# Kernel tuning notes

Hardware: AMD Instinct MI355X
Metric: run time of the kernel (lower is better)

## Reference

```python
import jax, jax.numpy as jnp
import numpy as np

K = 11  # masked conv3d kernel size

def mask_A(k):
    # mask type 'A': flattened (i,j,t) positions with current_id < k^3//2 + 1
    # (current_id starts at 1) -> first k^3//2 positions are 1.
    m = (np.arange(k ** 3) < (k ** 3) // 2).astype(np.float32).reshape(k, k, k)
    return jnp.asarray(m)

def conv3d(x, w, b, pad):
    out = jax.lax.conv_general_dilated(
        x, w, window_strides=(1, 1, 1), padding=[(pad, pad)] * 3,
        dimension_numbers=('NCDHW', 'OIDHW', 'NCDHW'))
    return out + b[None, :, None, None, None]

def conv2d(x, w, b, pad):
    out = jax.lax.conv_general_dilated(
        x, w, window_strides=(1, 1), padding=[(pad, pad)] * 2,
        dimension_numbers=('NCHW', 'OIHW', 'NCHW'))
    return out + b[None, :, None, None]

def pconv(x, w, b):
    # 1x1x1 conv3d as channel GEMM; w: [O, C]
    return jnp.einsum('bcdhw,oc->bodhw', x, w) + b[None, :, None, None, None]

def _phi(z):
    return 0.5 * (1.0 + jax.lax.erf(z / jnp.sqrt(2.0).astype(z.dtype)))

def setup_inputs() -> dict:
    key = jax.random.key(0)
    ks = jax.random.split(key, 12)
    M = 192
    B, H, W = 1, 48, 48
    s = 0.02
    x = jax.random.normal(ks[0], (B, M, H, W), jnp.float32)
    hyper = jax.random.normal(ks[1], (B, 2 * M, H, W), jnp.float32)
    W3 = s * jax.random.normal(ks[2], (M, 2 * M, 3, 3), jnp.float32)
    b3 = jnp.zeros((M,), jnp.float32)
    W1 = s * jax.random.normal(ks[3], (24, 1, K, K, K), jnp.float32)
    b1 = jnp.zeros((24,), jnp.float32)
    Wa = s * jax.random.normal(ks[4], (48, 25), jnp.float32)
    ba = jnp.zeros((48,), jnp.float32)
    Wb = s * jax.random.normal(ks[5], (96, 48), jnp.float32)
    bb = jnp.zeros((96,), jnp.float32)
    Wc = s * jax.random.normal(ks[6], (9, 96), jnp.float32)
    bc = jnp.zeros((9,), jnp.float32)
    return {"x": x, "hyper": hyper, "W3": W3, "b3": b3, "W1": W1, "b1": b1,
            "Wa": Wa, "ba": ba, "Wb": Wb, "bb": bb, "Wc": Wc, "bc": bc}

def reference(x, hyper, W3, b3, W1, b1, Wa, ba, Wb, bb, Wc, bc):
    # x: [B,M,H,W], hyper: [B,2M,H,W]
    x5 = x[:, None]                                   # [B,1,M,H,W]
    h = conv2d(hyper, W3, b3, 1)[:, None]             # [B,1,M,H,W]
    W1m = W1 * mask_A(K)[None, None]                  # causal mask re-applied each fwd
    x1 = conv3d(x5, W1m, b1, 5)                       # [B,24,M,H,W]
    t = jnp.concatenate([x1, h], axis=1)              # [B,25,M,H,W]
    t = jax.nn.relu(pconv(t, Wa, ba))                 # [B,48,M,H,W]
    t = jax.nn.relu(pconv(t, Wb, bb))                 # [B,96,M,H,W]
    out = pconv(t, Wc, bc)                            # [B,9,M,H,W]
    # 3-component weighted Gaussian entropy model
    mu = out[:, 0:3]
    sc = out[:, 3:6]
    sc = jnp.abs(jnp.where(sc == 0.0, 1e-9, sc))
    w = jax.nn.softmax(out[:, 6:9], axis=1)
    xe = x[:, None]                                   # [B,1,M,H,W]
    lik = jnp.abs(_phi((xe + 0.5 - mu) / sc) - _phi((xe - 0.5 - mu) / sc))
    p3 = jnp.sum(w * lik, axis=1)                     # [B,M,H,W]
    return (p3, out)
```

## Files before the change

### kernel.cpp

```cpp
#include <hip/hip_runtime.h>
#include <hip/hip_fp16.h>
#include <math.h>

#define HW    2304
#define NPOS  442368

typedef _Float16 f16x8 __attribute__((ext_vector_type(8)));
typedef __fp16   h16x2 __attribute__((ext_vector_type(2)));
typedef float    f32x4 __attribute__((ext_vector_type(4)));

__device__ __forceinline__ float phi_f(float z) {
    return 0.5f * (1.0f + erff(z * 0.70710678118654752f));
}
__device__ __forceinline__ unsigned short f2h(float v) {
    _Float16 h = (_Float16)v;
    return *reinterpret_cast<unsigned short*>(&h);
}
__device__ __forceinline__ unsigned int pk2(float a, float b) {
    return (unsigned int)f2h(a) | ((unsigned int)f2h(b) << 16);
}
__device__ __forceinline__ unsigned int pkrtz(float a, float b) {
    h16x2 h = __builtin_amdgcn_cvt_pkrtz(a, b);
    return *reinterpret_cast<unsigned int*>(&h);
}

__global__ __launch_bounds__(256) void prep_all(const float* __restrict__ hyper,
                                                const float* __restrict__ W3,
                                                const float* __restrict__ W1,
                                                const float* __restrict__ Wa,
                                                const float* __restrict__ ba,
                                                const float* __restrict__ b1,
                                                const float* __restrict__ Wb,
                                                const float* __restrict__ bb,
                                                const float* __restrict__ Wc,
                                                const float* __restrict__ xg,
                                                unsigned short* __restrict__ hyperTp,
                                                unsigned short* __restrict__ apack,
                                                unsigned short* __restrict__ pk,
                                                unsigned short* __restrict__ xhp) {
    const int bx = blockIdx.x;
    if (bx < 948) {
        __shared__ float s[32][33];
        const int pt = bx % 79, it = bx / 79;
        const int tid = threadIdx.x;
        const int c = tid & 31, r = tid >> 5;
        const int pp = pt * 32 + c;
        const int yp = pp / 50, xp = pp % 50;
        const bool inter = (pp < 2500) && yp >= 1 && yp <= 48 && xp >= 1 && xp <= 48;
        const int src = inter ? ((yp - 1) * 48 + (xp - 1)) : 0;
#pragma unroll
        for (int i = 0; i < 4; ++i) {
            int icl = r + i * 8;
            s[icl][c] = inter ? hyper[(size_t)(it * 32 + icl) * HW + src] : 0.f;
        }
        __syncthreads();
#pragma unroll
        for (int i = 0; i < 4; ++i) {
            int pl = r + i * 8;
            int pp2 = pt * 32 + pl;
            if (pp2 < 2500)
                hyperTp[(size_t)pp2 * 384 + it * 32 + c] = f2h(s[c][pl]);
        }
    } else if (bx < 3540) {
        int idx = (bx - 948) * 256 + threadIdx.x;
        int j = idx & 7;
        int l = (idx >> 3) & 63;
        int rest = idx >> 9;
        int t = rest % 9; rest /= 9;
        int c = rest % 12; int T = rest / 12;
        int oc = T * 16 + (l & 15);
        int ic = c * 32 + (l >> 4) * 8 + j;
        apack[idx] = f2h(W3[((size_t)oc * 384 + ic) * 9 + t]);
    } else if (bx < 3700) {
        int idx = (bx - 3540) * 256 + threadIdx.x;
        if (idx >= 40960) return;
        float v = 0.f;
        if (idx < 31744) {
            int j = idx & 7, lane = (idx >> 3) & 63, s = (idx >> 9) & 1, c = idx >> 10;
            int q = lane >> 4;
            int oc = s * 16 + (lane & 15);
            int r = 2 * c + (q >> 1), h = q & 1, kw = 8 * h + j;
            if (oc < 24 && r < 61 && kw < 11) {
                int kd = r / 11, kh = r % 11;
                int tap = kd * 121 + kh * 11 + kw;
                if (tap < 665) v = W1[oc * 1331 + tap];
            }
        } else if (idx < 33280) {
            int i2 = idx - 31744;
            int j = i2 & 7, lane = (i2 >> 3) & 63, t = i2 >> 9;
            int m = t * 16 + (lane & 15), k = (lane >> 4) * 8 + j;
            if (k < 25) v = Wa[m * 25 + k];
            else if (k == 25) {
                float s = ba[m];
                for (int c = 0; c < 24; ++c) s += Wa[m * 25 + c] * b1[c];
                v = s;
            }
        } else if (idx < 39424) {
            int i3 = idx - 33280;
            int j = i3 & 7, lane = (i3 >> 3) & 63, k2 = (i3 >> 9) & 1, s = i3 >> 10;
            int m = s * 16 + (lane & 15), ch = k2 * 32 + (lane >> 4) * 8 + j;
            if (ch < 48) v = Wb[m * 48 + ch];
            else if (ch == 48) v = bb[m];
        } else {
            int i4 = idx - 39424;
            int j = i4 & 7, lane = (i4 >> 3) & 63, k3 = i4 >> 9;
            int m = lane & 15, ch = k3 * 32 + (lane >> 4) * 8 + j;
            if (m < 9) v = Wc[m * 96 + ch];
        }
        pk[idx] = f2h(v);
    } else {
        int idx = (bx - 3700) * 256 + threadIdx.x;
        if (idx >= 187456) return;
        int si = idx * 4;
        int zp = si / 3712, rem = si - zp * 3712;
        int yp = rem >> 6, xp0 = rem & 63;
        float f[4];
#pragma unroll
        for (int k = 0; k < 4; ++k) {
            int xp = xp0 + k;
            bool in = zp >= 5 && zp < 197 && yp >= 5 && yp < 53 && xp >= 5 && xp < 53;
            f[k] = in ? xg[(size_t)(zp - 5) * HW + (yp - 5) * 48 + (xp - 5)] : 0.f;
        }
        *(uint2*)&xhp[si] = make_uint2(pk2(f[0], f[1]), pk2(f[2], f[3]));
    }
}

__global__ __launch_bounds__(256, 4) void fused3(const unsigned short* __restrict__ xhp,
                                                 const unsigned short* __restrict__ pk,
                                                 const unsigned short* __restrict__ hyperTp,
                                                 const unsigned short* __restrict__ apack,
                                                 const float* __restrict__ b3,
                                                 const float* __restrict__ xg,
                                                 const float* __restrict__ bc,
                                                 float* __restrict__ out) {
    __shared__ __align__(16) unsigned short P[6656];
    __shared__ __align__(16) unsigned short U[11264];
    __shared__ __align__(16) float htile[256];

    const int tid = threadIdx.x, w = tid >> 6, lane = tid & 63;
    const int n = lane & 15, q = lane >> 4;
    const int bx = blockIdx.x;
    const int x0 = (bx % 12) * 4, y0 = ((bx / 12) % 12) * 4;
    const int T = bx / 144, d0 = T * 16;

    float* hpart = (float*)U;

#pragma unroll
    for (int k = 0; k < 3; ++k) {
        int idx = tid + k * 256;
        if (idx < 588) {
            int row = idx >> 1, half = idx & 1;
            int py = row / 21, pz = row - py * 21;
            const uint4* src = (const uint4*)(xhp + ((size_t)(d0 + pz) * 58 + (y0 + py)) * 64
                                              + x0 + half * 8);
            *(uint4*)&P[row * 16 + half * 8] = *src;
        }
    }

    {
        f32x4 hacc = {0.f, 0.f, 0.f, 0.f};
        const int pp = (y0 + (n >> 2)) * 50 + x0 + (n & 3);
        const size_t bbase = (size_t)pp * 384 + q * 8;
#pragma unroll
        for (int cc = 0; cc < 3; ++cc) {
            const int c = w * 3 + cc;
            const unsigned short* ap = apack + ((size_t)(T * 12 + c) * 9) * 512 + lane * 8;
            const int coff = c * 32;
#pragma unroll
            for (int t = 0; t < 9; ++t) {
                f16x8 a = *(const f16x8*)(ap + t * 512);
                const int dd = (t / 3) * 50 + (t % 3);
                f16x8 b = *(const f16x8*)(hyperTp + bbase + (size_t)dd * 384 + coff);
                hacc = __builtin_amdgcn_mfma_f32_16x16x32_f16(a, b, hacc, 0, 0, 0);
            }
        }
#pragma unroll
        for (int e = 0; e < 4; ++e)
            hpart[w * 256 + (q * 4 + e) * 16 + n] = hacc[e];
    }
    __syncthreads();

    {
        const int oc = tid >> 4, pos = tid & 15;
        float h = b3[d0 + oc];
#pragma unroll
        for (int ww = 0; ww < 4; ++ww) h += hpart[ww * 256 + oc * 16 + pos];
        htile[oc * 16 + pos] = h;
    }

    const f32x4 zf = {0.f, 0.f, 0.f, 0.f};
    f32x4 acc[4][2];
#pragma unroll
    for (int p = 0; p < 4; ++p) { acc[p][0] = zf; acc[p][1] = zf; }

    const f16x8* Av = (const f16x8*)pk;
    const int par = q >> 1;
    const unsigned short* Pb = P + (w * 21 + n) * 16 + (q & 1) * 8;
#pragma unroll
    for (int c = 0; c < 31; ++c) {
        const int r0 = 2 * c, r1 = 2 * c + 1;
        const int o0 = ((r0 % 11) * 21 + (r0 / 11)) * 16;
        const int o1 = ((r1 % 11) * 21 + (r1 / 11)) * 16;
        const unsigned short* rp = Pb + (par ? o1 : o0);
        unsigned int u[6];
        *(uint4*)&u[0] = *(const uint4*)rp;
        *(uint2*)&u[4] = *(const uint2*)(rp + 8);
        f16x8 ca0 = Av[c * 128 + lane];
        f16x8 ca1 = Av[c * 128 + 64 + lane];
#pragma unroll
        for (int px = 0; px < 4; ++px) {
            unsigned int bw[4];
#pragma unroll
            for (int i = 0; i < 4; ++i) {
                if ((px & 1) == 0) bw[i] = u[(px >> 1) + i];
                else bw[i] = (u[(px >> 1) + i] >> 16) | (u[(px >> 1) + 1 + i] << 16);
            }
            f16x8 bf = *(f16x8*)bw;
            acc[px][0] = __builtin_amdgcn_mfma_f32_16x16x32_f16(ca0, bf, acc[px][0], 0, 0, 0);
            acc[px][1] = __builtin_amdgcn_mfma_f32_16x16x32_f16(ca1, bf, acc[px][1], 0, 0, 0);
        }
    }
    __syncthreads();

#pragma unroll
    for (int px = 0; px < 4; ++px) {
        unsigned int lo = pk2(acc[px][0][0], acc[px][0][1]);
        unsigned int hi = pk2(acc[px][0][2], acc[px][0][3]);
        *(uint2*)&P[(w * 16 + n) * 104 + px * 24 + q * 4] = make_uint2(lo, hi);
        if (q < 2) {
            unsigned int l2 = pk2(acc[px][1][0], acc[px][1][1]);
            unsigned int h2 = pk2(acc[px][1][2], acc[px][1][3]);
            *(uint2*)&P[(w * 16 + n) * 104 + px * 24 + 16 + q * 4] = make_uint2(l2, h2);
        }
    }

    const f16x8* WaF = (const f16x8*)(pk + 31744);
    const f16x8* WbF = (const f16x8*)(pk + 33280);
    const f16x8* WcF = (const f16x8*)(pk + 39424);
    f16x8 waf[3], wbf[12], wcf[3];
#pragma unroll
    for (int s = 0; s < 3; ++s) waf[s] = WaF[s * 64 + lane];
#pragma unroll
    for (int t = 0; t < 12; ++t) wbf[t] = WbF[t * 64 + lane];
#pragma unroll
    for (int k = 0; k < 3; ++k) wcf[k] = WcF[k * 64 + lane];
    float bcv[4];
#pragma unroll
    for (int e = 0; e < 4; ++e) bcv[e] = (q * 4 + e < 9) ? bc[q * 4 + e] : 0.f;

    unsigned short* t1w = U + w * 1152;
    unsigned short* t2w = U + 4608 + w * 1664;
    *(uint2*)&t1w[n * 72 + 48 + q * 4] = make_uint2((q == 0) ? 0x00003C00u : 0u, 0u);

    const f16x8 z8 = {};
    for (int px = 0; px < 4; ++px) {
        f16x8 b0;
        if (q < 3) {
            b0 = *(const f16x8*)&P[(w * 16 + n) * 104 + px * 24 + q * 8];
        } else {
            b0 = z8;
            b0[0] = (_Float16)htile[n * 16 + w * 4 + px];
            b0[1] = (_Float16)1.0f;
        }
#pragma unroll
        for (int s = 0; s < 3; ++s) {
            f32x4 r1 = __builtin_amdgcn_mfma_f32_16x16x32_f16(waf[s], b0, zf, 0, 0, 0);
            *(uint2*)&t1w[n * 72 + s * 16 + q * 4] =
                make_uint2(pkrtz(fmaxf(r1[0], 0.f), fmaxf(r1[1], 0.f)),
                           pkrtz(fmaxf(r1[2], 0.f), fmaxf(r1[3], 0.f)));
        }
        f32x4 rb[6];
#pragma unroll
        for (int s = 0; s < 6; ++s) rb[s] = zf;
#pragma unroll
        for (int k2 = 0; k2 < 2; ++k2) {
            f16x8 bf = *(const f16x8*)&t1w[n * 72 + k2 * 32 + q * 8];
#pragma unroll
            for (int s = 0; s < 6; ++s)
                rb[s] = __builtin_amdgcn_mfma_f32_16x16x32_f16(wbf[s * 2 + k2], bf, rb[s], 0, 0, 0);
        }
#pragma unroll
        for (int s = 0; s < 6; ++s)
            *(uint2*)&t2w[n * 104 + s * 16 + q * 4] =
                make_uint2(pkrtz(fmaxf(rb[s][0], 0.f), fmaxf(rb[s][1], 0.f)),
                           pkrtz(fmaxf(rb[s][2], 0.f), fmaxf(rb[s][3], 0.f)));
        f32x4 rc = zf;
#pragma unroll
        for (int k3 = 0; k3 < 3; ++k3) {
            f16x8 bf = *(const f16x8*)&t2w[n * 104 + k3 * 32 + q * 8];
            rc = __builtin_amdgcn_mfma_f32_16x16x32_f16(wcf[k3], bf, rc, 0, 0, 0);
        }
        {
            float* pr = (float*)(P + (w * 16 + n) * 104 + px * 24);
#pragma unroll
            for (int e = 0; e < 4; ++e) {
                const int row = q * 4 + e;
                if (row < 9) pr[row] = rc[e] + bcv[e];
            }
        }
    }

    {
        const float* pr = (const float*)(P + (w * 16 + (lane >> 2)) * 104 + (lane & 3) * 24);
        f32x4 oA = *(const f32x4*)pr;
        f32x4 oB = *(const f32x4*)(pr + 4);
        float o8 = pr[8];
        const int gp = (d0 + (lane >> 2)) * HW + (y0 + w) * 48 + x0 + (lane & 3);
        const float xv = xg[gp];
        float m = fmaxf(oB[2], fmaxf(oB[3], o8));
        float e0 = expf(oB[2] - m), e1 = expf(oB[3] - m), e2 = expf(o8 - m);
        float inv_es = 1.0f / (e0 + e1 + e2);
        float mu0 = oA[0], mu1 = oA[1], mu2 = oA[2];
        float s0 = oA[3], s1 = oB[0], s2 = oB[1];
        float p = 0.f;
#pragma unroll
        for (int jj = 0; jj < 3; ++jj) {
            float mu = (jj == 0) ? mu0 : (jj == 1) ? mu1 : mu2;
            float sc = (jj == 0) ? s0 : (jj == 1) ? s1 : s2;
            sc = (sc == 0.0f) ? 1e-9f : sc;
            sc = fabsf(sc);
            float a = phi_f((xv + 0.5f - mu) / sc);
            float b = phi_f((xv - 0.5f - mu) / sc);
            float lik = fabsf(a - b);
            float wgt = ((jj == 0) ? e0 : (jj == 1) ? e1 : e2) * inv_es;
            p = fmaf(wgt, lik, p);
        }
        out[gp] = p;
        out[NPOS + (size_t)0 * NPOS + gp] = mu0;
        out[NPOS + (size_t)1 * NPOS + gp] = mu1;
        out[NPOS + (size_t)2 * NPOS + gp] = mu2;
        out[NPOS + (size_t)3 * NPOS + gp] = s0;
        out[NPOS + (size_t)4 * NPOS + gp] = s1;
        out[NPOS + (size_t)5 * NPOS + gp] = s2;
        out[NPOS + (size_t)6 * NPOS + gp] = oB[2];
        out[NPOS + (size_t)7 * NPOS + gp] = oB[3];
        out[NPOS + (size_t)8 * NPOS + gp] = o8;
    }
}

extern "C" void kernel_launch(void* const* d_in, const int* in_sizes, int n_in,
                              void* d_out, int out_size, void* d_ws, size_t ws_size,
                              hipStream_t stream) {
    const float* x     = (const float*)d_in[0];
    const float* hyper = (const float*)d_in[1];
    const float* W3    = (const float*)d_in[2];
    const float* b3    = (const float*)d_in[3];
    const float* W1    = (const float*)d_in[4];
    const float* b1    = (const float*)d_in[5];
    const float* Wa    = (const float*)d_in[6];
    const float* ba    = (const float*)d_in[7];
    const float* Wb    = (const float*)d_in[8];
    const float* bb    = (const float*)d_in[9];
    const float* Wc    = (const float*)d_in[10];
    const float* bc    = (const float*)d_in[11];
    float* out = (float*)d_out;

    unsigned short* hyperTp = (unsigned short*)d_ws;
    unsigned short* apack   = hyperTp + 960000;
    unsigned short* pk      = apack + 663552;
    unsigned short* xhp     = pk + 40960;

    prep_all<<<4433, 256, 0, stream>>>(hyper, W3, W1, Wa, ba, b1, Wb, bb, Wc, x,
                                       hyperTp, apack, pk, xhp);
    fused3<<<1728, 256, 0, stream>>>(xhp, pk, hyperTp, apack, b3, x, bc, out);
}
```

Baseline: 151.8 us.

## Swizzle P tile, split hyper MFMA chains, and pass MLP activations via bpermute

The P tile halves are XOR-swizzled by row so the 128-bit and 64-bit LDS reads in the masked-conv loop spread across banks. The hyper conv uses three independent accumulator chains instead of one serial MFMA chain. The three pointwise MLP layers now move activations between MFMA output and input layouts with ds_bpermute in registers, so the t1/t2 scratch buffers and their LDS round-trips are gone and LDS use drops. The cost is extra bpermute and select instructions and higher register pressure.

```diff
diff --git a/kernel.cpp b/kernel.cpp
--- a/kernel.cpp
+++ b/kernel.cpp
@@ -22,6 +22,9 @@
 __device__ __forceinline__ unsigned int pkrtz(float a, float b) {
     h16x2 h = __builtin_amdgcn_cvt_pkrtz(a, b);
     return *reinterpret_cast<unsigned int*>(&h);
+}
+__device__ __forceinline__ unsigned int bperm(int idx4, unsigned int v) {
+    return (unsigned int)__builtin_amdgcn_ds_bpermute(idx4, (int)v);
 }
 
 __global__ __launch_bounds__(256) void prep_all(const float* __restrict__ hyper,
@@ -134,7 +137,7 @@
                                                  const float* __restrict__ bc,
                                                  float* __restrict__ out) {
     __shared__ __align__(16) unsigned short P[6656];
-    __shared__ __align__(16) unsigned short U[11264];
+    __shared__ __align__(16) float hpart[1024];
     __shared__ __align__(16) float htile[256];
 
     const int tid = threadIdx.x, w = tid >> 6, lane = tid & 63;
@@ -143,40 +146,41 @@
     const int x0 = (bx % 12) * 4, y0 = ((bx / 12) % 12) * 4;
     const int T = bx / 144, d0 = T * 16;
 
-    float* hpart = (float*)U;
-
 #pragma unroll
     for (int k = 0; k < 3; ++k) {
         int idx = tid + k * 256;
         if (idx < 588) {
             int row = idx >> 1, half = idx & 1;
             int py = row / 21, pz = row - py * 21;
+            int sw = (row >> 2) & 1;
             const uint4* src = (const uint4*)(xhp + ((size_t)(d0 + pz) * 58 + (y0 + py)) * 64
                                               + x0 + half * 8);
-            *(uint4*)&P[row * 16 + half * 8] = *src;
+            *(uint4*)&P[row * 16 + ((half ^ sw) << 3)] = *src;
         }
     }
 
     {
-        f32x4 hacc = {0.f, 0.f, 0.f, 0.f};
         const int pp = (y0 + (n >> 2)) * 50 + x0 + (n & 3);
         const size_t bbase = (size_t)pp * 384 + q * 8;
+        f32x4 hc[3];
 #pragma unroll
         for (int cc = 0; cc < 3; ++cc) {
             const int c = w * 3 + cc;
             const unsigned short* ap = apack + ((size_t)(T * 12 + c) * 9) * 512 + lane * 8;
             const int coff = c * 32;
+            f32x4 a0 = {0.f, 0.f, 0.f, 0.f};
 #pragma unroll
             for (int t = 0; t < 9; ++t) {
                 f16x8 a = *(const f16x8*)(ap + t * 512);
                 const int dd = (t / 3) * 50 + (t % 3);
                 f16x8 b = *(const f16x8*)(hyperTp + bbase + (size_t)dd * 384 + coff);
-                hacc = __builtin_amdgcn_mfma_f32_16x16x32_f16(a, b, hacc, 0, 0, 0);
-            }
+                a0 = __builtin_amdgcn_mfma_f32_16x16x32_f16(a, b, a0, 0, 0, 0);
+            }
+            hc[cc] = a0;
         }
 #pragma unroll
         for (int e = 0; e < 4; ++e)
-            hpart[w * 256 + (q * 4 + e) * 16 + n] = hacc[e];
+            hpart[w * 256 + (q * 4 + e) * 16 + n] = hc[0][e] + hc[1][e] + hc[2][e];
     }
     __syncthreads();
 
@@ -194,17 +198,20 @@
     for (int p = 0; p < 4; ++p) { acc[p][0] = zf; acc[p][1] = zf; }
 
     const f16x8* Av = (const f16x8*)pk;
-    const int par = q >> 1;
-    const unsigned short* Pb = P + (w * 21 + n) * 16 + (q & 1) * 8;
+    const int hb = q & 1, par = q >> 1;
+    const int w21n = w * 21 + n;
 #pragma unroll
     for (int c = 0; c < 31; ++c) {
         const int r0 = 2 * c, r1 = 2 * c + 1;
-        const int o0 = ((r0 % 11) * 21 + (r0 / 11)) * 16;
-        const int o1 = ((r1 % 11) * 21 + (r1 / 11)) * 16;
-        const unsigned short* rp = Pb + (par ? o1 : o0);
+        const int K0 = (r0 % 11) * 21 + (r0 / 11);
+        const int K1 = (r1 % 11) * 21 + (r1 / 11);
+        const int rowc = w21n + (par ? K1 : K0);
+        const int sw = (rowc >> 2) & 1;
+        const unsigned short* rp128 = P + rowc * 16 + ((hb ^ sw) << 3);
+        const unsigned short* rp64  = P + rowc * 16 + ((1  ^ sw) << 3);
         unsigned int u[6];
-        *(uint4*)&u[0] = *(const uint4*)rp;
-        *(uint2*)&u[4] = *(const uint2*)(rp + 8);
+        *(uint4*)&u[0] = *(const uint4*)rp128;
+        *(uint2*)&u[4] = *(const uint2*)rp64;
         f16x8 ca0 = Av[c * 128 + lane];
         f16x8 ca1 = Av[c * 128 + 64 + lane];
 #pragma unroll
@@ -248,9 +255,9 @@
 #pragma unroll
     for (int e = 0; e < 4; ++e) bcv[e] = (q * 4 + e < 9) ? bc[q * 4 + e] : 0.f;
 
-    unsigned short* t1w = U + w * 1152;
-    unsigned short* t2w = U + 4608 + w * 1664;
-    *(uint2*)&t1w[n * 72 + 48 + q * 4] = make_uint2((q == 0) ? 0x00003C00u : 0u, 0u);
+    const int idxg[2] = { (n + 16 * ((2 * q + 0) & 3)) * 4,
+                          (n + 16 * ((2 * q + 1) & 3)) * 4 };
+    const bool qlo = (q < 2);
 
     const f16x8 z8 = {};
     for (int px = 0; px < 4; ++px) {
@@ -262,33 +269,51 @@
             b0[0] = (_Float16)htile[n * 16 + w * 4 + px];
             b0[1] = (_Float16)1.0f;
         }
+        unsigned int pw1[6];
 #pragma unroll
         for (int s = 0; s < 3; ++s) {
             f32x4 r1 = __builtin_amdgcn_mfma_f32_16x16x32_f16(waf[s], b0, zf, 0, 0, 0);
-            *(uint2*)&t1w[n * 72 + s * 16 + q * 4] =
-                make_uint2(pkrtz(fmaxf(r1[0], 0.f), fmaxf(r1[1], 0.f)),
-                           pkrtz(fmaxf(r1[2], 0.f), fmaxf(r1[3], 0.f)));
-        }
-        f32x4 rb[6];
-#pragma unroll
-        for (int s = 0; s < 6; ++s) rb[s] = zf;
-#pragma unroll
-        for (int k2 = 0; k2 < 2; ++k2) {
-            f16x8 bf = *(const f16x8*)&t1w[n * 72 + k2 * 32 + q * 8];
-#pragma unroll
-            for (int s = 0; s < 6; ++s)
-                rb[s] = __builtin_amdgcn_mfma_f32_16x16x32_f16(wbf[s * 2 + k2], bf, rb[s], 0, 0, 0);
-        }
-#pragma unroll
-        for (int s = 0; s < 6; ++s)
-            *(uint2*)&t2w[n * 104 + s * 16 + q * 4] =
-                make_uint2(pkrtz(fmaxf(rb[s][0], 0.f), fmaxf(rb[s][1], 0.f)),
-                           pkrtz(fmaxf(rb[s][2], 0.f), fmaxf(rb[s][3], 0.f)));
+            pw1[s * 2 + 0] = pkrtz(fmaxf(r1[0], 0.f), fmaxf(r1[1], 0.f));
+            pw1[s * 2 + 1] = pkrtz(fmaxf(r1[2], 0.f), fmaxf(r1[3], 0.f));
+        }
+        unsigned int bpA[3][2][2];
+#pragma unroll
+        for (int s = 0; s < 3; ++s)
+#pragma unroll
+            for (int h = 0; h < 2; ++h) {
+                bpA[s][h][0] = bperm(idxg[0], pw1[s * 2 + h]);
+                bpA[s][h][1] = bperm(idxg[1], pw1[s * 2 + h]);
+            }
+        unsigned int bf0w[4], bf1w[4];
+#pragma unroll
+        for (int ww = 0; ww < 4; ++ww) {
+            const int h = ww & 1, g = ww >> 1;
+            bf0w[ww] = qlo ? bpA[0][h][g] : bpA[1][h][g];
+            unsigned int c1 = (q == 2) ? ((ww == 0) ? 0x00003C00u : 0u) : 0u;
+            bf1w[ww] = qlo ? bpA[2][h][g] : c1;
+        }
+        f16x8 bf0 = *(f16x8*)bf0w, bf1 = *(f16x8*)bf1w;
+        unsigned int pw2[12];
+#pragma unroll
+        for (int s = 0; s < 6; ++s) {
+            f32x4 rb = __builtin_amdgcn_mfma_f32_16x16x32_f16(wbf[s * 2 + 0], bf0, zf, 0, 0, 0);
+            rb = __builtin_amdgcn_mfma_f32_16x16x32_f16(wbf[s * 2 + 1], bf1, rb, 0, 0, 0);
+            pw2[s * 2 + 0] = pkrtz(fmaxf(rb[0], 0.f), fmaxf(rb[1], 0.f));
+            pw2[s * 2 + 1] = pkrtz(fmaxf(rb[2], 0.f), fmaxf(rb[3], 0.f));
+        }
         f32x4 rc = zf;
 #pragma unroll
         for (int k3 = 0; k3 < 3; ++k3) {
-            f16x8 bf = *(const f16x8*)&t2w[n * 104 + k3 * 32 + q * 8];
-            rc = __builtin_amdgcn_mfma_f32_16x16x32_f16(wcf[k3], bf, rc, 0, 0, 0);
+            unsigned int wv[4];
+#pragma unroll
+            for (int ww = 0; ww < 4; ++ww) {
+                const int h = ww & 1, g = ww >> 1;
+                unsigned int lo_ = bperm(idxg[g], pw2[(2 * k3) * 2 + h]);
+                unsigned int hi_ = bperm(idxg[g], pw2[(2 * k3 + 1) * 2 + h]);
+                wv[ww] = qlo ? lo_ : hi_;
+            }
+            f16x8 bfc = *(f16x8*)wv;
+            rc = __builtin_amdgcn_mfma_f32_16x16x32_f16(wcf[k3], bfc, rc, 0, 0, 0);
         }
         {
             float* pr = (float*)(P + (w * 16 + n) * 104 + px * 24);
```

Result: no change. 154.0 us (+1.4%).
